# Kernel optimization log

Measured on AMD Instinct MI355X. Metric: run time of the kernel, lower is better.

## Reference

```python
import jax, jax.numpy as jnp
import numpy as np


def setup_inputs() -> dict:
    key = jax.random.key(0)
    ks = jax.random.split(key, 8)
    h = 256
    b, o, T = 64, 64, 50
    s = 1.0 / np.sqrt(h)  # torch LSTM/Linear default init scale
    return {
        "x": jax.random.normal(ks[0], (b, o, h), dtype=jnp.float32),
        "W_ih": jax.random.uniform(ks[1], (4 * h, h), jnp.float32, -s, s),
        "W_hh": jax.random.uniform(ks[2], (4 * h, h), jnp.float32, -s, s),
        "b_ih": jax.random.uniform(ks[3], (4 * h,), jnp.float32, -s, s),
        "b_hh": jax.random.uniform(ks[4], (4 * h,), jnp.float32, -s, s),
        "c0": jnp.zeros((1, h), dtype=jnp.float32),
        "W_out": jax.random.uniform(ks[5], (h, h), jnp.float32, -s, s),
        "b_out": jax.random.uniform(ks[6], (h,), jnp.float32, -s, s),
        "sequence_length": T,
    }


def reference(x, W_ih, W_hh, b_ih, b_hh, c0, W_out, b_out, sequence_length):
    b, o, f = x.shape
    B = b * o
    h0 = x.reshape(B, f)                       # initial hidden state = input
    c_init = jnp.broadcast_to(c0, (B, f))      # learned initial cell state
    # Input token is constant across time: precompute input projection once.
    x_proj = h0 @ W_ih.T + b_ih + b_hh         # (B, 4f)

    def step(carry, _):
        hp, cp = carry
        gates = x_proj + hp @ W_hh.T           # (B, 4f), torch gate order i,f,g,o
        i_g, f_g, g_g, o_g = jnp.split(gates, 4, axis=-1)
        i_g = jax.nn.sigmoid(i_g)
        f_g = jax.nn.sigmoid(f_g)
        g_g = jnp.tanh(g_g)
        o_g = jax.nn.sigmoid(o_g)
        c = f_g * cp + i_g * g_g
        hn = o_g * jnp.tanh(c)
        return (hn, c), hn

    (_, _), hs = jax.lax.scan(step, (h0, c_init), None, length=sequence_length)
    # hs: (T, B, f) -> (b, o, T, f)
    hs = hs.transpose(1, 0, 2).reshape(b, o, sequence_length, f)
    return hs @ W_out.T + b_out
```

## Files before the change

### kernel.cpp

```cpp
#include <hip/hip_runtime.h>

typedef __attribute__((ext_vector_type(8))) short short8;
typedef __attribute__((ext_vector_type(4))) float f32x4;

#define F   256
#define SH  264

__device__ __forceinline__ short f2bf(float f) {
    union { float f; unsigned u; } v; v.f = f;
    unsigned r = (v.u + 0x7fffu + ((v.u >> 16) & 1u)) >> 16;
    return (short)r;
}
__device__ __forceinline__ float bf2f(short s) {
    union { float f; unsigned u; } v; v.u = ((unsigned)(unsigned short)s) << 16;
    return v.f;
}
__device__ __forceinline__ float sigm(float x) {
    return __builtin_amdgcn_rcpf(1.f + __builtin_amdgcn_exp2f(-1.442695041f * x));
}
__device__ __forceinline__ float tanhx(float x) {
    return 1.f - 2.f * __builtin_amdgcn_rcpf(1.f + __builtin_amdgcn_exp2f(2.885390082f * x));
}
__device__ __forceinline__ f32x4 splat4(float v) {
    f32x4 r; r[0] = v; r[1] = v; r[2] = v; r[3] = v; return r;
}

__global__ void pack_kernel(const float* __restrict__ Whh, const float* __restrict__ Wih,
                            const float* __restrict__ Wout,
                            short* __restrict__ whh_p, short* __restrict__ wih_hi,
                            short* __restrict__ wih_lo, short* __restrict__ wout_p)
{
    int idx = blockIdx.x * blockDim.x + threadIdx.x;
    if (idx < 64 * 8 * 64) {
        int lane = idx & 63, kt = (idx >> 6) & 7, nt = idx >> 9;
        int n = nt * 16 + (lane & 15);
        int k = kt * 32 + (lane >> 4) * 8;
        int w = (nt & 15) >> 1;
        int i = ((nt >> 4) << 1) | (nt & 1);
        int dst = (((w * 8 + kt) * 8 + i) * 64 + lane) * 8;
        const float* s1 = Whh + n * F + k;
        const float* s2 = Wih + n * F + k;
        #pragma unroll
        for (int j = 0; j < 8; j++) {
            whh_p[dst + j] = f2bf(s1[j]);
            float v = s2[j];
            short hi = f2bf(v);
            wih_hi[dst + j] = hi;
            wih_lo[dst + j] = f2bf(v - bf2f(hi));
        }
    } else {
        int i2 = idx - 64 * 8 * 64;
        if (i2 < 16 * 8 * 64) {
            int lane = i2 & 63, kt = (i2 >> 6) & 7, nt = i2 >> 9;
            int n = nt * 16 + (lane & 15);
            int k = kt * 32 + (lane >> 4) * 8;
            int w = nt >> 1, s = nt & 1;
            int dst = (((w * 8 + kt) * 2 + s) * 64 + lane) * 8;
            const float* sp = Wout + n * F + k;
            #pragma unroll
            for (int j = 0; j < 8; j++) wout_p[dst + j] = f2bf(sp[j]);
        }
    }
}

__device__ __forceinline__ void gate_mm(f32x4 (&acc)[8][2], const short* __restrict__ Wp,
                                        const short* hb, int lane)
{
    const int l15 = lane & 15, quad = lane >> 4;
    const short* bp = Wp + lane * 8;
    short8 be[8], bod[8];
    #pragma unroll
    for (int i = 0; i < 8; i++) be[i] = *(const short8*)(bp + i * 512);
    #pragma unroll
    for (int kt = 0; kt < 8; kt += 2) {
        #pragma unroll
        for (int i = 0; i < 8; i++)
            bod[i] = *(const short8*)(bp + (kt + 1) * 4096 + i * 512);
        short8 a0 = *(const short8*)(hb + l15 * SH + kt * 32 + quad * 8);
        short8 a1 = *(const short8*)(hb + (16 + l15) * SH + kt * 32 + quad * 8);
        #pragma unroll
        for (int i = 0; i < 8; i++) {
            acc[i][0] = __builtin_amdgcn_mfma_f32_16x16x32_bf16(a0, be[i], acc[i][0], 0, 0, 0);
            acc[i][1] = __builtin_amdgcn_mfma_f32_16x16x32_bf16(a1, be[i], acc[i][1], 0, 0, 0);
        }
        if (kt + 2 < 8) {
            #pragma unroll
            for (int i = 0; i < 8; i++)
                be[i] = *(const short8*)(bp + (kt + 2) * 4096 + i * 512);
        }
        a0 = *(const short8*)(hb + l15 * SH + (kt + 1) * 32 + quad * 8);
        a1 = *(const short8*)(hb + (16 + l15) * SH + (kt + 1) * 32 + quad * 8);
        #pragma unroll
        for (int i = 0; i < 8; i++) {
            acc[i][0] = __builtin_amdgcn_mfma_f32_16x16x32_bf16(a0, bod[i], acc[i][0], 0, 0, 0);
            acc[i][1] = __builtin_amdgcn_mfma_f32_16x16x32_bf16(a1, bod[i], acc[i][1], 0, 0, 0);
        }
    }
}

__global__ __launch_bounds__(512, 2)
void lstm_fused(const float* __restrict__ x, const float* __restrict__ b_ih,
                const float* __restrict__ b_hh, const float* __restrict__ c0,
                const float* __restrict__ b_out,
                const short* __restrict__ whh_p, const short* __restrict__ wih_hi,
                const short* __restrict__ wih_lo, const short* __restrict__ wout_p,
                const int* __restrict__ seqlen, float* __restrict__ out)
{
    __shared__ short hbuf[32 * SH];
    __shared__ short wout_lds[65536];
    const int T    = *seqlen;
    const int tid  = threadIdx.x;
    const int lane = tid & 63;
    const int w    = tid >> 6;
    const int l15  = lane & 15;
    const int quad = lane >> 4;
    const int row0 = blockIdx.x * 32;

    const short* whh_w    = whh_p  + (w << 15);
    const short* wih_hi_w = wih_hi + (w << 15);
    const short* wih_lo_w = wih_lo + (w << 15);

    {
        const short* src = wout_p + w * 8192 + lane * 8;
        short*       dst = wout_lds + w * 8192 + lane * 8;
        #pragma unroll
        for (int q = 0; q < 16; q++)
            *(short8*)(dst + q * 512) = *(const short8*)(src + q * 512);
    }

    const int xr = tid >> 4;
    const int xc = (tid & 15) * 16;
    float xv[16];
    {
        const float* xp = x + (size_t)(row0 + xr) * F + xc;
        #pragma unroll
        for (int j = 0; j < 16; j++) xv[j] = xp[j];
    }

    f32x4 xpj[8][2];
    #pragma unroll
    for (int i = 0; i < 8; i++) { xpj[i][0] = splat4(0.f); xpj[i][1] = splat4(0.f); }

    #pragma unroll
    for (int j = 0; j < 16; j++) {
        short hi = f2bf(xv[j]);
        hbuf[xr * SH + xc + j] = f2bf(xv[j] - bf2f(hi));
    }
    __syncthreads();
    gate_mm(xpj, wih_hi_w, hbuf, lane);
    __syncthreads();
    #pragma unroll
    for (int j = 0; j < 16; j++) hbuf[xr * SH + xc + j] = f2bf(xv[j]);
    __syncthreads();
    gate_mm(xpj, wih_hi_w, hbuf, lane);
    gate_mm(xpj, wih_lo_w, hbuf, lane);

    #pragma unroll
    for (int i = 0; i < 8; i++) {
        int nt = (i >> 1) * 16 + 2 * w + (i & 1);
        float bias = b_ih[nt * 16 + l15] + b_hh[nt * 16 + l15];
        #pragma unroll
        for (int mt = 0; mt < 2; mt++)
            #pragma unroll
            for (int r = 0; r < 4; r++) xpj[i][mt][r] += bias;
    }

    float cst[2][2][4];
    float bo[2];
    #pragma unroll
    for (int s = 0; s < 2; s++) {
        float cv = c0[w * 32 + s * 16 + l15];
        bo[s]    = b_out[w * 32 + s * 16 + l15];
        #pragma unroll
        for (int mt = 0; mt < 2; mt++)
            #pragma unroll
            for (int r = 0; r < 4; r++) cst[s][mt][r] = cv;
    }

    const size_t orow = (size_t)T * F;
    const short* wl = wout_lds + w * 8192 + lane * 8;

    for (int t = 0; t < T; t++) {
        f32x4 acc[8][2];
        #pragma unroll
        for (int i = 0; i < 8; i++) { acc[i][0] = xpj[i][0]; acc[i][1] = xpj[i][1]; }
        gate_mm(acc, whh_w, hbuf, lane);

        __syncthreads();

        #pragma unroll
        for (int s = 0; s < 2; s++)
          #pragma unroll
          for (int mt = 0; mt < 2; mt++)
            #pragma unroll
            for (int r = 0; r < 4; r++) {
                float ig = sigm(acc[0 + s][mt][r]);
                float fg = sigm(acc[2 + s][mt][r]);
                float gg = tanhx(acc[4 + s][mt][r]);
                float og = sigm(acc[6 + s][mt][r]);
                float c  = fg * cst[s][mt][r] + ig * gg;
                cst[s][mt][r] = c;
                hbuf[(mt * 16 + quad * 4 + r) * SH + w * 32 + s * 16 + l15]
                    = f2bf(og * tanhx(c));
            }
        __syncthreads();

        f32x4 oacc[2][2];
        #pragma unroll
        for (int s = 0; s < 2; s++) { oacc[s][0] = splat4(bo[s]); oacc[s][1] = splat4(bo[s]); }
        #pragma unroll
        for (int kt = 0; kt < 8; kt++) {
            short8 a0 = *(const short8*)(hbuf + l15 * SH + kt * 32 + quad * 8);
            short8 a1 = *(const short8*)(hbuf + (16 + l15) * SH + kt * 32 + quad * 8);
            #pragma unroll
            for (int s = 0; s < 2; s++) {
                short8 b = *(const short8*)(wl + kt * 1024 + s * 512);
                oacc[s][0] = __builtin_amdgcn_mfma_f32_16x16x32_bf16(a0, b, oacc[s][0], 0, 0, 0);
                oacc[s][1] = __builtin_amdgcn_mfma_f32_16x16x32_bf16(a1, b, oacc[s][1], 0, 0, 0);
            }
        }
        float* op = out + (size_t)row0 * orow + (size_t)t * F;
        #pragma unroll
        for (int s = 0; s < 2; s++)
          #pragma unroll
          for (int mt = 0; mt < 2; mt++)
            #pragma unroll
            for (int r = 0; r < 4; r++)
                __builtin_nontemporal_store(
                    oacc[s][mt][r],
                    &op[(size_t)(mt * 16 + quad * 4 + r) * orow + w * 32 + s * 16 + l15]);
    }
}

extern "C" void kernel_launch(void* const* d_in, const int* in_sizes, int n_in,
                              void* d_out, int out_size, void* d_ws, size_t ws_size,
                              hipStream_t stream)
{
    const float* x    = (const float*)d_in[0];
    const float* Wih  = (const float*)d_in[1];
    const float* Whh  = (const float*)d_in[2];
    const float* bih  = (const float*)d_in[3];
    const float* bhh  = (const float*)d_in[4];
    const float* c0   = (const float*)d_in[5];
    const float* Wout = (const float*)d_in[6];
    const float* bout = (const float*)d_in[7];
    const int* seqlen = (const int*)d_in[8];

    short* whh_p  = (short*)d_ws;
    short* wih_hi = whh_p  + 1024 * 256;
    short* wih_lo = wih_hi + 1024 * 256;
    short* wout_p = wih_lo + 1024 * 256;
    (void)ws_size; (void)in_sizes; (void)n_in; (void)out_size;

    pack_kernel<<<160, 256, 0, stream>>>(Whh, Wih, Wout, whh_p, wih_hi, wih_lo, wout_p);
    lstm_fused<<<128, 512, 0, stream>>>(x, bih, bhh, c0, bout,
                                        whh_p, wih_hi, wih_lo, wout_p,
                                        seqlen, (float*)d_out);
}
```

Before: 1.018 ms.

## Split output projection out of recurrent LSTM kernel into separate GEMM kernel

When workspace allows, the recurrent kernel now only writes bf16 hidden states to a global buffer, and a separate out_proj kernel computes the output projection with 512 blocks and Wout held in registers. This takes the per-step output MFMA work and the strided output stores off the serial critical path of the 128-block recurrence, and frees the 128 KB Wout LDS footprint. In exchange it adds an extra global round trip of the hidden states and a second launch, and it falls back to the fused kernel if the workspace is too small.

Result: no change. 1.031 ms (+1.3%).

```diff
diff --git a/kernel.cpp b/kernel.cpp
--- a/kernel.cpp
+++ b/kernel.cpp
@@ -98,16 +98,18 @@
     }
 }
 
+template<int FUSED>
 __global__ __launch_bounds__(512, 2)
-void lstm_fused(const float* __restrict__ x, const float* __restrict__ b_ih,
-                const float* __restrict__ b_hh, const float* __restrict__ c0,
-                const float* __restrict__ b_out,
-                const short* __restrict__ whh_p, const short* __restrict__ wih_hi,
-                const short* __restrict__ wih_lo, const short* __restrict__ wout_p,
-                const int* __restrict__ seqlen, float* __restrict__ out)
+void lstm_ker(const float* __restrict__ x, const float* __restrict__ b_ih,
+              const float* __restrict__ b_hh, const float* __restrict__ c0,
+              const float* __restrict__ b_out,
+              const short* __restrict__ whh_p, const short* __restrict__ wih_hi,
+              const short* __restrict__ wih_lo, const short* __restrict__ wout_p,
+              const int* __restrict__ seqlen, short* __restrict__ G,
+              float* __restrict__ out)
 {
     __shared__ short hbuf[32 * SH];
-    __shared__ short wout_lds[65536];
+    __shared__ short wout_lds[FUSED ? 65536 : 8];
     const int T    = *seqlen;
     const int tid  = threadIdx.x;
     const int lane = tid & 63;
@@ -120,7 +122,7 @@
     const short* wih_hi_w = wih_hi + (w << 15);
     const short* wih_lo_w = wih_lo + (w << 15);
 
-    {
+    if (FUSED) {
         const short* src = wout_p + w * 8192 + lane * 8;
         short*       dst = wout_lds + w * 8192 + lane * 8;
         #pragma unroll
@@ -179,6 +181,7 @@
 
     const size_t orow = (size_t)T * F;
     const short* wl = wout_lds + w * 8192 + lane * 8;
+    const int dxc = (tid & 15) * 8;
 
     for (int t = 0; t < T; t++) {
         f32x4 acc[8][2];
@@ -205,21 +208,87 @@
             }
         __syncthreads();
 
+        if (!FUSED) {
+            short* gp = G + ((size_t)(row0 + xr) * T + t) * F;
+            short8 h0 = *(const short8*)(hbuf + xr * SH + dxc);
+            short8 h1 = *(const short8*)(hbuf + xr * SH + 128 + dxc);
+            __builtin_nontemporal_store(h0, (short8*)(gp + dxc));
+            __builtin_nontemporal_store(h1, (short8*)(gp + 128 + dxc));
+        } else {
+            f32x4 oacc[2][2];
+            #pragma unroll
+            for (int s = 0; s < 2; s++) { oacc[s][0] = splat4(bo[s]); oacc[s][1] = splat4(bo[s]); }
+            #pragma unroll
+            for (int kt = 0; kt < 8; kt++) {
+                short8 a0 = *(const short8*)(hbuf + l15 * SH + kt * 32 + quad * 8);
+                short8 a1 = *(const short8*)(hbuf + (16 + l15) * SH + kt * 32 + quad * 8);
+                #pragma unroll
+                for (int s = 0; s < 2; s++) {
+                    short8 b = *(const short8*)(wl + kt * 1024 + s * 512);
+                    oacc[s][0] = __builtin_amdgcn_mfma_f32_16x16x32_bf16(a0, b, oacc[s][0], 0, 0, 0);
+                    oacc[s][1] = __builtin_amdgcn_mfma_f32_16x16x32_bf16(a1, b, oacc[s][1], 0, 0, 0);
+                }
+            }
+            float* op = out + (size_t)row0 * orow + (size_t)t * F;
+            #pragma unroll
+            for (int s = 0; s < 2; s++)
+              #pragma unroll
+              for (int mt = 0; mt < 2; mt++)
+                #pragma unroll
+                for (int r = 0; r < 4; r++)
+                    __builtin_nontemporal_store(
+                        oacc[s][mt][r],
+                        &op[(size_t)(mt * 16 + quad * 4 + r) * orow + w * 32 + s * 16 + l15]);
+        }
+    }
+}
+
+__global__ __launch_bounds__(512, 4)
+void out_proj(const short* __restrict__ G, const short* __restrict__ wout_p,
+              const float* __restrict__ b_out, const int* __restrict__ seqlen,
+              float* __restrict__ out)
+{
+    __shared__ short abuf[32 * SH];
+    const int M    = 4096 * (*seqlen);
+    const int tid  = threadIdx.x;
+    const int lane = tid & 63;
+    const int w    = tid >> 6;
+    const int l15  = lane & 15;
+    const int quad = lane >> 4;
+    const int xr   = tid >> 4;
+    const int xc   = (tid & 15) * 16;
+
+    short8 wb[2][8];
+    #pragma unroll
+    for (int s = 0; s < 2; s++)
+        #pragma unroll
+        for (int kt = 0; kt < 8; kt++)
+            wb[s][kt] = *(const short8*)(wout_p + w * 8192 + kt * 1024 + s * 512 + lane * 8);
+
+    float bo[2] = { b_out[w * 32 + l15], b_out[w * 32 + 16 + l15] };
+
+    for (int ch = blockIdx.x; ch * 32 < M; ch += gridDim.x) {
+        const int m0 = ch * 32;
+        const short* gp = G + (size_t)(m0 + xr) * F + xc;
+        *(short8*)(abuf + xr * SH + xc)     = *(const short8*)(gp);
+        *(short8*)(abuf + xr * SH + xc + 8) = *(const short8*)(gp + 8);
+        __syncthreads();
+
         f32x4 oacc[2][2];
         #pragma unroll
         for (int s = 0; s < 2; s++) { oacc[s][0] = splat4(bo[s]); oacc[s][1] = splat4(bo[s]); }
         #pragma unroll
         for (int kt = 0; kt < 8; kt++) {
-            short8 a0 = *(const short8*)(hbuf + l15 * SH + kt * 32 + quad * 8);
-            short8 a1 = *(const short8*)(hbuf + (16 + l15) * SH + kt * 32 + quad * 8);
+            short8 a0 = *(const short8*)(abuf + l15 * SH + kt * 32 + quad * 8);
+            short8 a1 = *(const short8*)(abuf + (16 + l15) * SH + kt * 32 + quad * 8);
             #pragma unroll
             for (int s = 0; s < 2; s++) {
-                short8 b = *(const short8*)(wl + kt * 1024 + s * 512);
-                oacc[s][0] = __builtin_amdgcn_mfma_f32_16x16x32_bf16(a0, b, oacc[s][0], 0, 0, 0);
-                oacc[s][1] = __builtin_amdgcn_mfma_f32_16x16x32_bf16(a1, b, oacc[s][1], 0, 0, 0);
+                oacc[s][0] = __builtin_amdgcn_mfma_f32_16x16x32_bf16(a0, wb[s][kt], oacc[s][0], 0, 0, 0);
+                oacc[s][1] = __builtin_amdgcn_mfma_f32_16x16x32_bf16(a1, wb[s][kt], oacc[s][1], 0, 0, 0);
             }
         }
-        float* op = out + (size_t)row0 * orow + (size_t)t * F;
+
+        float* op = out + (size_t)m0 * F;
         #pragma unroll
         for (int s = 0; s < 2; s++)
           #pragma unroll
@@ -228,7 +297,8 @@
             for (int r = 0; r < 4; r++)
                 __builtin_nontemporal_store(
                     oacc[s][mt][r],
-                    &op[(size_t)(mt * 16 + quad * 4 + r) * orow + w * 32 + s * 16 + l15]);
+                    &op[(size_t)(mt * 16 + quad * 4 + r) * F + w * 32 + s * 16 + l15]);
+        __syncthreads();
     }
 }
 
@@ -246,14 +316,26 @@
     const float* bout = (const float*)d_in[7];
     const int* seqlen = (const int*)d_in[8];
 
-    short* whh_p  = (short*)d_ws;
-    short* wih_hi = whh_p  + 1024 * 256;
-    short* wih_lo = wih_hi + 1024 * 256;
-    short* wout_p = wih_lo + 1024 * 256;
-    (void)ws_size; (void)in_sizes; (void)n_in; (void)out_size;
+    char* ws = (char*)d_ws;
+    short* whh_p  = (short*)(ws);
+    short* wih_hi = (short*)(ws + 512 * 1024);
+    short* wih_lo = (short*)(ws + 1024 * 1024);
+    short* wout_p = (short*)(ws + 1536 * 1024);
+    short* G      = (short*)(ws + 1664 * 1024);
+    (void)in_sizes; (void)n_in;
+
+    const size_t need = 1664 * 1024 + (size_t)out_size * 2;
 
     pack_kernel<<<160, 256, 0, stream>>>(Whh, Wih, Wout, whh_p, wih_hi, wih_lo, wout_p);
-    lstm_fused<<<128, 512, 0, stream>>>(x, bih, bhh, c0, bout,
-                                        whh_p, wih_hi, wih_lo, wout_p,
-                                        seqlen, (float*)d_out);
-}
+
+    if (ws_size >= need) {
+        lstm_ker<0><<<128, 512, 0, stream>>>(x, bih, bhh, c0, bout,
+                                             whh_p, wih_hi, wih_lo, wout_p,
+                                             seqlen, G, (float*)d_out);
+        out_proj<<<512, 512, 0, stream>>>(G, wout_p, bout, seqlen, (float*)d_out);
+    } else {
+        lstm_ker<1><<<128, 512, 0, stream>>>(x, bih, bhh, c0, bout,
+                                             whh_p, wih_hi, wih_lo, wout_p,
+                                             seqlen, G, (float*)d_out);
+    }
+}
```
